# Performance work log

Measured on AMD Instinct MI355X. Metric: run time of the kernel, lower is better.

## Reference

```python
import jax, jax.numpy as jnp
import numpy as np

D_MODEL = 1024
N_HEAD = 16
HEAD_DIM = D_MODEL // N_HEAD


def setup_inputs() -> dict:
    key = jax.random.key(0)
    k1, k2, k3 = jax.random.split(key, 3)
    B, T = 2, 2048
    x = jax.random.normal(k1, (B, T, D_MODEL), dtype=jnp.float32)
    # nn.MultiheadAttention packed in-projection: (3*D, D), xavier-like scale
    w_in = jax.random.normal(k2, (3 * D_MODEL, D_MODEL), dtype=jnp.float32) * (1.0 / np.sqrt(D_MODEL))
    b_in = jnp.zeros((3 * D_MODEL,), dtype=jnp.float32)
    w_out = jax.random.normal(k3, (D_MODEL, D_MODEL), dtype=jnp.float32) * (1.0 / np.sqrt(D_MODEL))
    b_out = jnp.zeros((D_MODEL,), dtype=jnp.float32)
    return {"x": x, "w_in": w_in, "b_in": b_in, "w_out": w_out, "b_out": b_out}


def reference(x, w_in, b_in, w_out, b_out):
    B, T, D = x.shape
    H, hd = N_HEAD, HEAD_DIM
    # packed QKV projection (torch Linear convention: y = x @ W.T + b)
    qkv = x @ w_in.T + b_in                      # [B, T, 3D]
    q, k, v = jnp.split(qkv, 3, axis=-1)
    # [B, H, T, hd]
    q = q.reshape(B, T, H, hd).transpose(0, 2, 1, 3)
    k = k.reshape(B, T, H, hd).transpose(0, 2, 1, 3)
    v = v.reshape(B, T, H, hd).transpose(0, 2, 1, 3)
    scale = 1.0 / np.sqrt(hd).astype(np.float32)
    scores = jnp.einsum("bhqd,bhkd->bhqk", q * scale, k)  # [B, H, T, T]
    causal = jnp.tril(jnp.ones((T, T), dtype=bool))
    scores = jnp.where(causal, scores, jnp.finfo(scores.dtype).min)
    attn = jax.nn.softmax(scores, axis=-1)
    ctx = jnp.einsum("bhqk,bhkd->bhqd", attn, v)           # [B, H, T, hd]
    ctx = ctx.transpose(0, 2, 1, 3).reshape(B, T, D)
    return ctx @ w_out.T + b_out
```

## Files before the change

### kernel.cpp

```cpp
#include <hip/hip_runtime.h>


#define T_SEQ 2048
#define D_MODEL 1024
#define NEG_BIG (-1.0e30f)
#define Q_SCALE 0.18033688f

typedef float f32x4 __attribute__((ext_vector_type(4)));
typedef short s16x8 __attribute__((ext_vector_type(8)));
typedef __bf16 bf16x8 __attribute__((ext_vector_type(8)));

__device__ __forceinline__ f32x4 mfma16(s16x8 a, s16x8 b, f32x4 c) {
    return __builtin_amdgcn_mfma_f32_16x16x32_bf16(
        __builtin_bit_cast(bf16x8, a), __builtin_bit_cast(bf16x8, b), c, 0, 0, 0);
}

__device__ __forceinline__ short f2bf(float f) {
    unsigned int u = __float_as_uint(f);
    u += 0x7fffu + ((u >> 16) & 1u);
    return (short)(u >> 16);
}
__device__ __forceinline__ unsigned f2bfu(float f) {
    unsigned int u = __float_as_uint(f);
    u += 0x7fffu + ((u >> 16) & 1u);
    return u >> 16;
}
__device__ __forceinline__ unsigned f2bfu_fast(float f) {
    return (__float_as_uint(f) + 0x8000u) >> 16;
}
__device__ __forceinline__ float bf2f(short s) {
    return __uint_as_float(((unsigned int)(unsigned short)s) << 16);
}

__device__ __forceinline__ void async_lds16(const short* g, short* l) {
    __builtin_amdgcn_global_load_lds(
        (const __attribute__((address_space(1))) unsigned int*)g,
        (__attribute__((address_space(3))) unsigned int*)l, 16, 0, 0);
}

#define N_X   4194304
#define N_WI  3145728
#define N_BI  3072
#define N_WO  1048576
#define N_BO  1024
#define V_X   (N_X  / 4)
#define V_WI  (N_WI / 4)
#define V_BI  (N_BI / 4)
#define V_WO  (N_WO / 4)
#define V_BO  (N_BO / 4)
#define V_TOT (V_X + V_WI + V_BI + V_WO + V_BO)

__global__ __launch_bounds__(256) void canon_all_kernel(
    const float* __restrict__ x, const float* __restrict__ wi,
    const float* __restrict__ bi, const float* __restrict__ wo,
    const float* __restrict__ bo,
    short* __restrict__ xb, short* __restrict__ wib, short* __restrict__ bib,
    short* __restrict__ wob, short* __restrict__ bob)
{
    int i = blockIdx.x * 256 + threadIdx.x;
    if (i >= V_TOT) return;
    const float* src; short* dst; int off;
    if      (i < V_X)                    { src = x;  dst = xb;  off = i; }
    else if (i < V_X+V_WI)               { src = wi; dst = wib; off = i - V_X; }
    else if (i < V_X+V_WI+V_BI)          { src = bi; dst = bib; off = i - V_X - V_WI; }
    else if (i < V_X+V_WI+V_BI+V_WO)     { src = wo; dst = wob; off = i - V_X - V_WI - V_BI; }
    else                                 { src = bo; dst = bob; off = i - V_X - V_WI - V_BI - V_WO; }
    float4 v = ((const float4*)src)[off];
    short4 o = { f2bf(v.x), f2bf(v.y), f2bf(v.z), f2bf(v.w) };
    ((short4*)dst)[off] = o;
}

__global__ __launch_bounds__(256) void gemm_qkv_kernel(
    const short* __restrict__ A, const short* __restrict__ B,
    const short* __restrict__ bias,
    short* __restrict__ qo, short* __restrict__ ko, short* __restrict__ vt)
{
    const int K = 1024;
    alignas(16) __shared__ short As[128][32];
    alignas(16) __shared__ short Bs[128][32];
    const int m0 = blockIdx.x * 128;
    const int n0 = blockIdx.y * 128;
    const int tid = threadIdx.x;
    const int lane = tid & 63;
    const int w = tid >> 6;
    const int wm = (w >> 1) * 64, wn = (w & 1) * 64;
    const int quad = lane >> 4, l16 = lane & 15;

    f32x4 acc[4][4];
    const f32x4 zero = {0.f, 0.f, 0.f, 0.f};
#pragma unroll
    for (int i = 0; i < 4; ++i)
#pragma unroll
        for (int j = 0; j < 4; ++j) acc[i][j] = zero;

    const int lrow = lane >> 2;
    const int lcol = (lane & 3) * 8;
    const short* gA0 = &A[(m0 + w*32      + lrow) * K + lcol];
    const short* gA1 = &A[(m0 + w*32 + 16 + lrow) * K + lcol];
    const short* gB0 = &B[(n0 + w*32      + lrow) * K + lcol];
    const short* gB1 = &B[(n0 + w*32 + 16 + lrow) * K + lcol];
    short* lA0 = &As[w*32][0];
    short* lA1 = &As[w*32 + 16][0];
    short* lB0 = &Bs[w*32][0];
    short* lB1 = &Bs[w*32 + 16][0];

    for (int k0 = 0; k0 < K; k0 += 32) {
        __syncthreads();
        async_lds16(gA0 + k0, lA0);
        async_lds16(gA1 + k0, lA1);
        async_lds16(gB0 + k0, lB0);
        async_lds16(gB1 + k0, lB1);
        __syncthreads();

        s16x8 af[4], bfr[4];
#pragma unroll
        for (int i = 0; i < 4; ++i) af[i]  = *(const s16x8*)&As[wm + i*16 + l16][quad*8];
#pragma unroll
        for (int j = 0; j < 4; ++j) bfr[j] = *(const s16x8*)&Bs[wn + j*16 + l16][quad*8];
#pragma unroll
        for (int i = 0; i < 4; ++i)
#pragma unroll
            for (int j = 0; j < 4; ++j)
                acc[i][j] = mfma16(af[i], bfr[j], acc[i][j]);
    }

#pragma unroll
    for (int j = 0; j < 4; ++j) {
        int n = n0 + wn + j*16 + l16;
        float bi = bf2f(bias[n]);
        int which = n >> 10;
        int h = (n >> 6) & 15, d = n & 63;
        if (which == 2) {
#pragma unroll
            for (int i = 0; i < 4; ++i) {
                int tb = m0 + wm + i*16 + quad*4;
                int b = tb >> 11, t = tb & 2047;
                uint2 pk;
                pk.x = f2bfu(acc[i][j][0] + bi) | (f2bfu(acc[i][j][1] + bi) << 16);
                pk.y = f2bfu(acc[i][j][2] + bi) | (f2bfu(acc[i][j][3] + bi) << 16);
                *(uint2*)&vt[(((size_t)(b*16 + h)) * 64 + d) * 2048 + t] = pk;
            }
        } else {
            short* dst = (which == 0) ? qo : ko;
            float scl = (which == 0) ? Q_SCALE : 1.0f;
#pragma unroll
            for (int i = 0; i < 4; ++i) {
#pragma unroll
                for (int r = 0; r < 4; ++r) {
                    int m = m0 + wm + i*16 + quad*4 + r;
                    int b = m >> 11, t = m & 2047;
                    float v = (acc[i][j][r] + bi) * scl;
                    dst[(((b*16 + h) * 2048) + t) * 64 + d] = f2bf(v);
                }
            }
        }
    }
}

__global__ __launch_bounds__(256) void attn_kernel(
    const short* __restrict__ Q, const short* __restrict__ K,
    const short* __restrict__ Vt, short* __restrict__ ctx)
{
    alignas(16) __shared__ short Ks[64][72];
    alignas(16) __shared__ short Vs[64][72];
    alignas(16) __shared__ short Pl[4][16][72];

    const int bh = blockIdx.x;
    const int qt = 31 - (int)blockIdx.y;
    const int qbase = qt * 64;
    const int tid = threadIdx.x;
    const int w = tid >> 6, lane = tid & 63;
    const int quad = lane >> 4, l16 = lane & 15;
    const int b = bh >> 4, h = bh & 15;

    const short* Qb  = Q  + bh * T_SEQ * 64;
    const short* Kb  = K  + bh * T_SEQ * 64;
    const short* Vbt = Vt + bh * 64 * T_SEQ;

    const short* qrow = Qb + (qbase + w*16 + l16) * 64;
    const s16x8 qa0 = *(const s16x8*)(qrow + quad*8);
    const s16x8 qa1 = *(const s16x8*)(qrow + 32 + quad*8);

    const f32x4 zero = {0.f, 0.f, 0.f, 0.f};
    f32x4 o[4];
#pragma unroll
    for (int dt = 0; dt < 4; ++dt) o[dt] = zero;
    float lsum = 0.f;

    const int sr  = tid >> 3;
    const int scl = (tid & 7) * 8;
    const int qg  = qbase + w*16 + l16;

    for (int s0 = 0; s0 <= qbase; s0 += 64) {
        __syncthreads();
        *(float4*)&Ks[sr][scl]    = *(const float4*)&Kb[(s0 + sr) * 64 + scl];
        *(float4*)&Ks[sr+32][scl] = *(const float4*)&Kb[(s0 + sr + 32) * 64 + scl];
        *(float4*)&Vs[sr][scl]    = *(const float4*)&Vbt[(size_t)sr * T_SEQ + s0 + scl];
        *(float4*)&Vs[sr+32][scl] = *(const float4*)&Vbt[(size_t)(sr + 32) * T_SEQ + s0 + scl];
        __syncthreads();

#pragma unroll
        for (int sub = 0; sub < 4; ++sub) {
            s16x8 ka0 = *(const s16x8*)&Ks[sub*16 + l16][quad*8];
            s16x8 ka1 = *(const s16x8*)&Ks[sub*16 + l16][32 + quad*8];
            f32x4 S = mfma16(ka1, qa1, mfma16(ka0, qa0, zero));
            if (s0 == qbase) {
                int sb = s0 + sub*16 + quad*4;
#pragma unroll
                for (int r = 0; r < 4; ++r)
                    if (sb + r > qg) S[r] = NEG_BIG;
            }
            float p0 = exp2f(S[0]), p1 = exp2f(S[1]);
            float p2 = exp2f(S[2]), p3 = exp2f(S[3]);
            lsum += (p0 + p1) + (p2 + p3);
            uint2 pk;
            pk.x = f2bfu_fast(p0) | (f2bfu_fast(p1) << 16);
            pk.y = f2bfu_fast(p2) | (f2bfu_fast(p3) << 16);
            *(uint2*)&Pl[w][l16][sub*16 + quad*4] = pk;
        }

        s16x8 pb0 = *(const s16x8*)&Pl[w][l16][quad*8];
        s16x8 pb1 = *(const s16x8*)&Pl[w][l16][32 + quad*8];
#pragma unroll
        for (int dt = 0; dt < 4; ++dt) {
            s16x8 va0 = *(const s16x8*)&Vs[dt*16 + l16][quad*8];
            s16x8 va1 = *(const s16x8*)&Vs[dt*16 + l16][32 + quad*8];
            o[dt] = mfma16(va1, pb1, mfma16(va0, pb0, o[dt]));
        }
    }

    lsum += __shfl_xor(lsum, 16, 64);
    lsum += __shfl_xor(lsum, 32, 64);
    float inv = 1.0f / lsum;
    int base = (b * T_SEQ + qg) * D_MODEL + h * 64;
#pragma unroll
    for (int dt = 0; dt < 4; ++dt) {
        uint2 pk;
        pk.x = f2bfu(o[dt][0] * inv) | (f2bfu(o[dt][1] * inv) << 16);
        pk.y = f2bfu(o[dt][2] * inv) | (f2bfu(o[dt][3] * inv) << 16);
        *(uint2*)&ctx[base + dt*16 + quad*4] = pk;
    }
}

__global__ __launch_bounds__(256) void gemm_out_kernel(
    const short* __restrict__ A, const short* __restrict__ B,
    const short* __restrict__ bias, float* __restrict__ out)
{
    const int K = 1024;
    alignas(16) __shared__ short As[128][32];
    alignas(16) __shared__ short Bs[64][32];
    const int m0 = blockIdx.x * 128;
    const int n0 = blockIdx.y * 64;
    const int tid = threadIdx.x;
    const int lane = tid & 63;
    const int w = tid >> 6;
    const int wm = (w >> 1) * 64, wn = (w & 1) * 32;
    const int quad = lane >> 4, l16 = lane & 15;

    f32x4 acc[4][2];
    const f32x4 zero = {0.f, 0.f, 0.f, 0.f};
#pragma unroll
    for (int i = 0; i < 4; ++i)
#pragma unroll
        for (int j = 0; j < 2; ++j) acc[i][j] = zero;

    const int lrow = lane >> 2;
    const int lcol = (lane & 3) * 8;
    const short* gA0 = &A[(m0 + w*32      + lrow) * K + lcol];
    const short* gA1 = &A[(m0 + w*32 + 16 + lrow) * K + lcol];
    const short* gB0 = &B[(n0 + w*16      + lrow) * K + lcol];
    short* lA0 = &As[w*32][0];
    short* lA1 = &As[w*32 + 16][0];
    short* lB0 = &Bs[w*16][0];

    for (int k0 = 0; k0 < K; k0 += 32) {
        __syncthreads();
        async_lds16(gA0 + k0, lA0);
        async_lds16(gA1 + k0, lA1);
        async_lds16(gB0 + k0, lB0);
        __syncthreads();

        s16x8 af[4], bfr[2];
#pragma unroll
        for (int i = 0; i < 4; ++i) af[i]  = *(const s16x8*)&As[wm + i*16 + l16][quad*8];
#pragma unroll
        for (int j = 0; j < 2; ++j) bfr[j] = *(const s16x8*)&Bs[wn + j*16 + l16][quad*8];
#pragma unroll
        for (int i = 0; i < 4; ++i)
#pragma unroll
            for (int j = 0; j < 2; ++j)
                acc[i][j] = mfma16(af[i], bfr[j], acc[i][j]);
    }

#pragma unroll
    for (int j = 0; j < 2; ++j) {
        int n = n0 + wn + j*16 + l16;
        float bi = bf2f(bias[n]);
#pragma unroll
        for (int i = 0; i < 4; ++i) {
#pragma unroll
            for (int r = 0; r < 4; ++r) {
                int m = m0 + wm + i*16 + quad*4 + r;
                out[m * 1024 + n] = acc[i][j][r] + bi;
            }
        }
    }
}

extern "C" void kernel_launch(void* const* d_in, const int* in_sizes, int n_in,
                              void* d_out, int out_size, void* d_ws, size_t ws_size,
                              hipStream_t stream) {
    float* out = (float*)d_out;
    char* ws = (char*)d_ws;

    const size_t MB = 1u << 20;
    short* xb     = (short*)(ws);
    short* w_inb  = (short*)(ws + 8*MB);
    short* b_inb  = (short*)(ws + 14*MB);
    short* w_outb = (short*)(ws + 15*MB);
    short* b_outb = (short*)(ws + 17*MB);
    short* qb     = (short*)(ws + 18*MB);
    short* kb     = (short*)(ws + 26*MB);
    short* vtb    = (short*)(ws + 34*MB);
    short* ctxb   = (short*)(ws + 42*MB);

    canon_all_kernel<<<(V_TOT + 255) / 256, 256, 0, stream>>>(
        (const float*)d_in[0], (const float*)d_in[1], (const float*)d_in[2],
        (const float*)d_in[3], (const float*)d_in[4],
        xb, w_inb, b_inb, w_outb, b_outb);

    gemm_qkv_kernel<<<dim3(32, 24), 256, 0, stream>>>(xb, w_inb, b_inb, qb, kb, vtb);
    attn_kernel<<<dim3(32, 32), 256, 0, stream>>>(qb, kb, vtb, ctxb);
    gemm_out_kernel<<<dim3(32, 16), 256, 0, stream>>>(ctxb, w_outb, b_outb, out);
}
```

Before: 195.8 us.

## Process two query tiles per attention block and transpose V in separate kernel

The attention kernel now handles 128 query rows per block as two 64-row sub-tiles. Each K/V tile loaded into shared memory is reused by both sub-tiles, which halves the K/V global loads and the number of blocks. The QKV GEMM now writes V in the same row-major layout as Q and K, and a new transpose kernel builds V^T, reusing the x bf16 buffer, to replace the strided transposed store. The costs are an extra kernel launch and an extra pass over V, more registers per thread, and coarser causal work balance with fewer blocks.

```diff
diff --git a/kernel.cpp b/kernel.cpp
--- a/kernel.cpp
+++ b/kernel.cpp
@@ -73,7 +73,7 @@
 __global__ __launch_bounds__(256) void gemm_qkv_kernel(
     const short* __restrict__ A, const short* __restrict__ B,
     const short* __restrict__ bias,
-    short* __restrict__ qo, short* __restrict__ ko, short* __restrict__ vt)
+    short* __restrict__ qo, short* __restrict__ ko, short* __restrict__ vo)
 {
     const int K = 1024;
     alignas(16) __shared__ short As[128][32];
@@ -129,32 +129,46 @@
         int n = n0 + wn + j*16 + l16;
         float bi = bf2f(bias[n]);
         int which = n >> 10;
+        short* dst = (which == 0) ? qo : (which == 1) ? ko : vo;
+        float scl = (which == 0) ? Q_SCALE : 1.0f;
         int h = (n >> 6) & 15, d = n & 63;
-        if (which == 2) {
-#pragma unroll
-            for (int i = 0; i < 4; ++i) {
-                int tb = m0 + wm + i*16 + quad*4;
-                int b = tb >> 11, t = tb & 2047;
-                uint2 pk;
-                pk.x = f2bfu(acc[i][j][0] + bi) | (f2bfu(acc[i][j][1] + bi) << 16);
-                pk.y = f2bfu(acc[i][j][2] + bi) | (f2bfu(acc[i][j][3] + bi) << 16);
-                *(uint2*)&vt[(((size_t)(b*16 + h)) * 64 + d) * 2048 + t] = pk;
+#pragma unroll
+        for (int i = 0; i < 4; ++i) {
+#pragma unroll
+            for (int r = 0; r < 4; ++r) {
+                int m = m0 + wm + i*16 + quad*4 + r;
+                int b = m >> 11, t = m & 2047;
+                float v = (acc[i][j][r] + bi) * scl;
+                dst[(((b*16 + h) * 2048) + t) * 64 + d] = f2bf(v);
             }
-        } else {
-            short* dst = (which == 0) ? qo : ko;
-            float scl = (which == 0) ? Q_SCALE : 1.0f;
-#pragma unroll
-            for (int i = 0; i < 4; ++i) {
-#pragma unroll
-                for (int r = 0; r < 4; ++r) {
-                    int m = m0 + wm + i*16 + quad*4 + r;
-                    int b = m >> 11, t = m & 2047;
-                    float v = (acc[i][j][r] + bi) * scl;
-                    dst[(((b*16 + h) * 2048) + t) * 64 + d] = f2bf(v);
-                }
-            }
-        }
-    }
+        }
+    }
+}
+
+__global__ __launch_bounds__(256) void transpose_v_kernel(
+    const short* __restrict__ V, short* __restrict__ Vt)
+{
+    alignas(16) __shared__ short buf[64][72];
+    const int bh = blockIdx.x;
+    const int t0 = blockIdx.y * 64;
+    const int tid = threadIdx.x;
+    const int r = tid >> 2;
+    const int c = (tid & 3) * 16;
+
+    const short* src = V + ((size_t)bh * T_SEQ + t0) * 64;
+    *(float4*)&buf[r][c]     = *(const float4*)&src[r * 64 + c];
+    *(float4*)&buf[r][c + 8] = *(const float4*)&src[r * 64 + c + 8];
+    __syncthreads();
+
+    s16x8 o0, o1;
+#pragma unroll
+    for (int k2 = 0; k2 < 8; ++k2) {
+        o0[k2] = buf[c + k2][r];
+        o1[k2] = buf[c + 8 + k2][r];
+    }
+    short* dst = Vt + ((size_t)bh * 64 + r) * T_SEQ + t0;
+    *(s16x8*)&dst[c]     = o0;
+    *(s16x8*)&dst[c + 8] = o1;
 }
 
 __global__ __launch_bounds__(256) void attn_kernel(
@@ -163,11 +177,11 @@
 {
     alignas(16) __shared__ short Ks[64][72];
     alignas(16) __shared__ short Vs[64][72];
-    alignas(16) __shared__ short Pl[4][16][72];
+    alignas(16) __shared__ short Pl[4][32][72];
 
     const int bh = blockIdx.x;
-    const int qt = 31 - (int)blockIdx.y;
-    const int qbase = qt * 64;
+    const int qt = 15 - (int)blockIdx.y;
+    const int qbase = qt * 128;
     const int tid = threadIdx.x;
     const int w = tid >> 6, lane = tid & 63;
     const int quad = lane >> 4, l16 = lane & 15;
@@ -175,70 +189,101 @@
 
     const short* Qb  = Q  + bh * T_SEQ * 64;
     const short* Kb  = K  + bh * T_SEQ * 64;
-    const short* Vbt = Vt + bh * 64 * T_SEQ;
-
-    const short* qrow = Qb + (qbase + w*16 + l16) * 64;
-    const s16x8 qa0 = *(const s16x8*)(qrow + quad*8);
-    const s16x8 qa1 = *(const s16x8*)(qrow + 32 + quad*8);
+    const short* Vbt = Vt + (size_t)bh * 64 * T_SEQ;
+
+    s16x8 qa0[2], qa1[2];
+#pragma unroll
+    for (int qs = 0; qs < 2; ++qs) {
+        const short* qrow = Qb + (qbase + qs*64 + w*16 + l16) * 64;
+        qa0[qs] = *(const s16x8*)(qrow + quad*8);
+        qa1[qs] = *(const s16x8*)(qrow + 32 + quad*8);
+    }
 
     const f32x4 zero = {0.f, 0.f, 0.f, 0.f};
-    f32x4 o[4];
-#pragma unroll
-    for (int dt = 0; dt < 4; ++dt) o[dt] = zero;
-    float lsum = 0.f;
-
-    const int sr  = tid >> 3;
-    const int scl = (tid & 7) * 8;
-    const int qg  = qbase + w*16 + l16;
-
-    for (int s0 = 0; s0 <= qbase; s0 += 64) {
-        __syncthreads();
-        *(float4*)&Ks[sr][scl]    = *(const float4*)&Kb[(s0 + sr) * 64 + scl];
-        *(float4*)&Ks[sr+32][scl] = *(const float4*)&Kb[(s0 + sr + 32) * 64 + scl];
-        *(float4*)&Vs[sr][scl]    = *(const float4*)&Vbt[(size_t)sr * T_SEQ + s0 + scl];
-        *(float4*)&Vs[sr+32][scl] = *(const float4*)&Vbt[(size_t)(sr + 32) * T_SEQ + s0 + scl];
-        __syncthreads();
-
+    f32x4 o[2][4];
+#pragma unroll
+    for (int qs = 0; qs < 2; ++qs)
+#pragma unroll
+        for (int dt = 0; dt < 4; ++dt) o[qs][dt] = zero;
+    float lsum[2] = {0.f, 0.f};
+
+    const int sr = tid >> 2;
+    const int sc = (tid & 3) * 16;
+
+    for (int s0 = 0; s0 <= qbase + 64; s0 += 64) {
+        __syncthreads();
+        *(float4*)&Ks[sr][sc]     = *(const float4*)&Kb[(s0 + sr) * 64 + sc];
+        *(float4*)&Ks[sr][sc + 8] = *(const float4*)&Kb[(s0 + sr) * 64 + sc + 8];
+        *(float4*)&Vs[sr][sc]     = *(const float4*)&Vbt[(size_t)sr * T_SEQ + s0 + sc];
+        *(float4*)&Vs[sr][sc + 8] = *(const float4*)&Vbt[(size_t)sr * T_SEQ + s0 + sc + 8];
+        __syncthreads();
+
+        const bool f0 = (s0 <= qbase);
+
+        s16x8 ka0[4], ka1[4];
 #pragma unroll
         for (int sub = 0; sub < 4; ++sub) {
-            s16x8 ka0 = *(const s16x8*)&Ks[sub*16 + l16][quad*8];
-            s16x8 ka1 = *(const s16x8*)&Ks[sub*16 + l16][32 + quad*8];
-            f32x4 S = mfma16(ka1, qa1, mfma16(ka0, qa0, zero));
-            if (s0 == qbase) {
-                int sb = s0 + sub*16 + quad*4;
-#pragma unroll
-                for (int r = 0; r < 4; ++r)
-                    if (sb + r > qg) S[r] = NEG_BIG;
+            ka0[sub] = *(const s16x8*)&Ks[sub*16 + l16][quad*8];
+            ka1[sub] = *(const s16x8*)&Ks[sub*16 + l16][32 + quad*8];
+        }
+
+#pragma unroll
+        for (int qs = 0; qs < 2; ++qs) {
+            if (qs == 0 && !f0) continue;
+            const int fqb = qbase + qs*64;
+            const int qg = fqb + w*16 + l16;
+#pragma unroll
+            for (int sub = 0; sub < 4; ++sub) {
+                f32x4 S = mfma16(ka1[sub], qa1[qs], mfma16(ka0[sub], qa0[qs], zero));
+                if (s0 == fqb) {
+                    int sb = s0 + sub*16 + quad*4;
+#pragma unroll
+                    for (int r = 0; r < 4; ++r)
+                        if (sb + r > qg) S[r] = NEG_BIG;
+                }
+                float p0 = exp2f(S[0]), p1 = exp2f(S[1]);
+                float p2 = exp2f(S[2]), p3 = exp2f(S[3]);
+                lsum[qs] += (p0 + p1) + (p2 + p3);
+                uint2 pk;
+                pk.x = f2bfu_fast(p0) | (f2bfu_fast(p1) << 16);
+                pk.y = f2bfu_fast(p2) | (f2bfu_fast(p3) << 16);
+                *(uint2*)&Pl[w][qs*16 + l16][sub*16 + quad*4] = pk;
             }
-            float p0 = exp2f(S[0]), p1 = exp2f(S[1]);
-            float p2 = exp2f(S[2]), p3 = exp2f(S[3]);
-            lsum += (p0 + p1) + (p2 + p3);
+        }
+
+        s16x8 va0[4], va1[4];
+#pragma unroll
+        for (int dt = 0; dt < 4; ++dt) {
+            va0[dt] = *(const s16x8*)&Vs[dt*16 + l16][quad*8];
+            va1[dt] = *(const s16x8*)&Vs[dt*16 + l16][32 + quad*8];
+        }
+
+#pragma unroll
+        for (int qs = 0; qs < 2; ++qs) {
+            if (qs == 0 && !f0) continue;
+            s16x8 pb0 = *(const s16x8*)&Pl[w][qs*16 + l16][quad*8];
+            s16x8 pb1 = *(const s16x8*)&Pl[w][qs*16 + l16][32 + quad*8];
+#pragma unroll
+            for (int dt = 0; dt < 4; ++dt)
+                o[qs][dt] = mfma16(va1[dt], pb1, mfma16(va0[dt], pb0, o[qs][dt]));
+        }
+    }
+
+#pragma unroll
+    for (int qs = 0; qs < 2; ++qs) {
+        float l = lsum[qs];
+        l += __shfl_xor(l, 16, 64);
+        l += __shfl_xor(l, 32, 64);
+        float inv = 1.0f / l;
+        int qg = qbase + qs*64 + w*16 + l16;
+        int base = (b * T_SEQ + qg) * D_MODEL + h * 64;
+#pragma unroll
+        for (int dt = 0; dt < 4; ++dt) {
             uint2 pk;
-            pk.x = f2bfu_fast(p0) | (f2bfu_fast(p1) << 16);
-            pk.y = f2bfu_fast(p2) | (f2bfu_fast(p3) << 16);
-            *(uint2*)&Pl[w][l16][sub*16 + quad*4] = pk;
-        }
-
-        s16x8 pb0 = *(const s16x8*)&Pl[w][l16][quad*8];
-        s16x8 pb1 = *(const s16x8*)&Pl[w][l16][32 + quad*8];
-#pragma unroll
-        for (int dt = 0; dt < 4; ++dt) {
-            s16x8 va0 = *(const s16x8*)&Vs[dt*16 + l16][quad*8];
-            s16x8 va1 = *(const s16x8*)&Vs[dt*16 + l16][32 + quad*8];
-            o[dt] = mfma16(va1, pb1, mfma16(va0, pb0, o[dt]));
-        }
-    }
-
-    lsum += __shfl_xor(lsum, 16, 64);
-    lsum += __shfl_xor(lsum, 32, 64);
-    float inv = 1.0f / lsum;
-    int base = (b * T_SEQ + qg) * D_MODEL + h * 64;
-#pragma unroll
-    for (int dt = 0; dt < 4; ++dt) {
-        uint2 pk;
-        pk.x = f2bfu(o[dt][0] * inv) | (f2bfu(o[dt][1] * inv) << 16);
-        pk.y = f2bfu(o[dt][2] * inv) | (f2bfu(o[dt][3] * inv) << 16);
-        *(uint2*)&ctx[base + dt*16 + quad*4] = pk;
+            pk.x = f2bfu(o[qs][dt][0] * inv) | (f2bfu(o[qs][dt][1] * inv) << 16);
+            pk.y = f2bfu(o[qs][dt][2] * inv) | (f2bfu(o[qs][dt][3] * inv) << 16);
+            *(uint2*)&ctx[base + dt*16 + quad*4] = pk;
+        }
     }
 }
 
@@ -321,15 +366,17 @@
     short* b_outb = (short*)(ws + 17*MB);
     short* qb     = (short*)(ws + 18*MB);
     short* kb     = (short*)(ws + 26*MB);
-    short* vtb    = (short*)(ws + 34*MB);
+    short* vb     = (short*)(ws + 34*MB);
     short* ctxb   = (short*)(ws + 42*MB);
+    short* vtb    = xb;
 
     canon_all_kernel<<<(V_TOT + 255) / 256, 256, 0, stream>>>(
         (const float*)d_in[0], (const float*)d_in[1], (const float*)d_in[2],
         (const float*)d_in[3], (const float*)d_in[4],
         xb, w_inb, b_inb, w_outb, b_outb);
 
-    gemm_qkv_kernel<<<dim3(32, 24), 256, 0, stream>>>(xb, w_inb, b_inb, qb, kb, vtb);
-    attn_kernel<<<dim3(32, 32), 256, 0, stream>>>(qb, kb, vtb, ctxb);
+    gemm_qkv_kernel<<<dim3(32, 24), 256, 0, stream>>>(xb, w_inb, b_inb, qb, kb, vb);
+    transpose_v_kernel<<<dim3(32, 32), 256, 0, stream>>>(vb, vtb);
+    attn_kernel<<<dim3(32, 16), 256, 0, stream>>>(qb, kb, vtb, ctxb);
     gemm_out_kernel<<<dim3(32, 16), 256, 0, stream>>>(ctxb, w_outb, b_outb, out);
 }
```

Result: no change. 199.3 us (+1.7%).

## Transpose V in a separate kernel and register-prefetch K/V tiles in attention

Applied to the files above, without the earlier changes.

The QKV GEMM now writes V in the same row-major head layout as Q and K, replacing the scattered transposed 8-byte stores. A new LDS-based transpose kernel builds Vt, reusing the xb workspace buffer. In the attention kernel, the next K/V tile is loaded into registers while the current tile is computed, so global latency overlaps with MFMA work. This adds a kernel launch and an extra pass over V, and the prefetch raises register pressure.

```diff
diff --git a/kernel.cpp b/kernel.cpp
--- a/kernel.cpp
+++ b/kernel.cpp
@@ -73,7 +73,7 @@
 __global__ __launch_bounds__(256) void gemm_qkv_kernel(
     const short* __restrict__ A, const short* __restrict__ B,
     const short* __restrict__ bias,
-    short* __restrict__ qo, short* __restrict__ ko, short* __restrict__ vt)
+    short* __restrict__ qo, short* __restrict__ ko, short* __restrict__ vo)
 {
     const int K = 1024;
     alignas(16) __shared__ short As[128][32];
@@ -129,32 +129,46 @@
         int n = n0 + wn + j*16 + l16;
         float bi = bf2f(bias[n]);
         int which = n >> 10;
+        short* dst = (which == 0) ? qo : (which == 1) ? ko : vo;
+        float scl = (which == 0) ? Q_SCALE : 1.0f;
         int h = (n >> 6) & 15, d = n & 63;
-        if (which == 2) {
-#pragma unroll
-            for (int i = 0; i < 4; ++i) {
-                int tb = m0 + wm + i*16 + quad*4;
-                int b = tb >> 11, t = tb & 2047;
-                uint2 pk;
-                pk.x = f2bfu(acc[i][j][0] + bi) | (f2bfu(acc[i][j][1] + bi) << 16);
-                pk.y = f2bfu(acc[i][j][2] + bi) | (f2bfu(acc[i][j][3] + bi) << 16);
-                *(uint2*)&vt[(((size_t)(b*16 + h)) * 64 + d) * 2048 + t] = pk;
+#pragma unroll
+        for (int i = 0; i < 4; ++i) {
+#pragma unroll
+            for (int r = 0; r < 4; ++r) {
+                int m = m0 + wm + i*16 + quad*4 + r;
+                int b = m >> 11, t = m & 2047;
+                float v = (acc[i][j][r] + bi) * scl;
+                dst[(((b*16 + h) * 2048) + t) * 64 + d] = f2bf(v);
             }
-        } else {
-            short* dst = (which == 0) ? qo : ko;
-            float scl = (which == 0) ? Q_SCALE : 1.0f;
-#pragma unroll
-            for (int i = 0; i < 4; ++i) {
-#pragma unroll
-                for (int r = 0; r < 4; ++r) {
-                    int m = m0 + wm + i*16 + quad*4 + r;
-                    int b = m >> 11, t = m & 2047;
-                    float v = (acc[i][j][r] + bi) * scl;
-                    dst[(((b*16 + h) * 2048) + t) * 64 + d] = f2bf(v);
-                }
-            }
-        }
-    }
+        }
+    }
+}
+
+__global__ __launch_bounds__(256) void transpose_v_kernel(
+    const short* __restrict__ V, short* __restrict__ Vt)
+{
+    alignas(16) __shared__ short buf[64][72];
+    const int bh = blockIdx.x;
+    const int t0 = blockIdx.y * 64;
+    const int tid = threadIdx.x;
+    const int r = tid >> 2;
+    const int c = (tid & 3) * 16;
+
+    const short* src = V + ((size_t)bh * T_SEQ + t0) * 64;
+    *(float4*)&buf[r][c]     = *(const float4*)&src[r * 64 + c];
+    *(float4*)&buf[r][c + 8] = *(const float4*)&src[r * 64 + c + 8];
+    __syncthreads();
+
+    s16x8 o0, o1;
+#pragma unroll
+    for (int k2 = 0; k2 < 8; ++k2) {
+        o0[k2] = buf[c + k2][r];
+        o1[k2] = buf[c + 8 + k2][r];
+    }
+    short* dst = Vt + ((size_t)bh * 64 + r) * T_SEQ + t0;
+    *(s16x8*)&dst[c]     = o0;
+    *(s16x8*)&dst[c + 8] = o1;
 }
 
 __global__ __launch_bounds__(256) void attn_kernel(
@@ -175,7 +189,7 @@
 
     const short* Qb  = Q  + bh * T_SEQ * 64;
     const short* Kb  = K  + bh * T_SEQ * 64;
-    const short* Vbt = Vt + bh * 64 * T_SEQ;
+    const short* Vbt = Vt + (size_t)bh * 64 * T_SEQ;
 
     const short* qrow = Qb + (qbase + w*16 + l16) * 64;
     const s16x8 qa0 = *(const s16x8*)(qrow + quad*8);
@@ -191,13 +205,25 @@
     const int scl = (tid & 7) * 8;
     const int qg  = qbase + w*16 + l16;
 
+    float4 kf0 = *(const float4*)&Kb[sr * 64 + scl];
+    float4 kf1 = *(const float4*)&Kb[(sr + 32) * 64 + scl];
+    float4 vf0 = *(const float4*)&Vbt[(size_t)sr * T_SEQ + scl];
+    float4 vf1 = *(const float4*)&Vbt[(size_t)(sr + 32) * T_SEQ + scl];
+
     for (int s0 = 0; s0 <= qbase; s0 += 64) {
         __syncthreads();
-        *(float4*)&Ks[sr][scl]    = *(const float4*)&Kb[(s0 + sr) * 64 + scl];
-        *(float4*)&Ks[sr+32][scl] = *(const float4*)&Kb[(s0 + sr + 32) * 64 + scl];
-        *(float4*)&Vs[sr][scl]    = *(const float4*)&Vbt[(size_t)sr * T_SEQ + s0 + scl];
-        *(float4*)&Vs[sr+32][scl] = *(const float4*)&Vbt[(size_t)(sr + 32) * T_SEQ + s0 + scl];
-        __syncthreads();
+        *(float4*)&Ks[sr][scl]    = kf0;
+        *(float4*)&Ks[sr+32][scl] = kf1;
+        *(float4*)&Vs[sr][scl]    = vf0;
+        *(float4*)&Vs[sr+32][scl] = vf1;
+        __syncthreads();
+
+        if (s0 + 64 <= qbase) {
+            kf0 = *(const float4*)&Kb[(s0 + 64 + sr) * 64 + scl];
+            kf1 = *(const float4*)&Kb[(s0 + 64 + sr + 32) * 64 + scl];
+            vf0 = *(const float4*)&Vbt[(size_t)sr * T_SEQ + s0 + 64 + scl];
+            vf1 = *(const float4*)&Vbt[(size_t)(sr + 32) * T_SEQ + s0 + 64 + scl];
+        }
 
 #pragma unroll
         for (int sub = 0; sub < 4; ++sub) {
@@ -268,7 +294,7 @@
     const int lcol = (lane & 3) * 8;
     const short* gA0 = &A[(m0 + w*32      + lrow) * K + lcol];
     const short* gA1 = &A[(m0 + w*32 + 16 + lrow) * K + lcol];
-    const short* gB0 = &B[(n0 + w*16      + lrow) * K + lcol];
+    const short* gB0 = &B[(n0 + w*16 + lrow) * K + lcol];
     short* lA0 = &As[w*32][0];
     short* lA1 = &As[w*32 + 16][0];
     short* lB0 = &Bs[w*16][0];
@@ -321,15 +347,17 @@
     short* b_outb = (short*)(ws + 17*MB);
     short* qb     = (short*)(ws + 18*MB);
     short* kb     = (short*)(ws + 26*MB);
-    short* vtb    = (short*)(ws + 34*MB);
+    short* vb     = (short*)(ws + 34*MB);
     short* ctxb   = (short*)(ws + 42*MB);
+    short* vtb    = xb;
 
     canon_all_kernel<<<(V_TOT + 255) / 256, 256, 0, stream>>>(
         (const float*)d_in[0], (const float*)d_in[1], (const float*)d_in[2],
         (const float*)d_in[3], (const float*)d_in[4],
         xb, w_inb, b_inb, w_outb, b_outb);
 
-    gemm_qkv_kernel<<<dim3(32, 24), 256, 0, stream>>>(xb, w_inb, b_inb, qb, kb, vtb);
+    gemm_qkv_kernel<<<dim3(32, 24), 256, 0, stream>>>(xb, w_inb, b_inb, qb, kb, vb);
+    transpose_v_kernel<<<dim3(32, 32), 256, 0, stream>>>(vb, vtb);
     attn_kernel<<<dim3(32, 32), 256, 0, stream>>>(qb, kb, vtb, ctxb);
     gemm_out_kernel<<<dim3(32, 16), 256, 0, stream>>>(ctxb, w_outb, b_outb, out);
 }
```

After: 181.9 us. 1.08x faster.
